# Kernel tuning notes

Hardware: AMD Instinct MI355X
Metric: run time of the kernel (lower is better)

The kernel has to match this reference:

```python
import jax, jax.numpy as jnp
import numpy as np

N, J, H, O, SD = 6144, 2000, 100, 6144, 2


def setup_inputs() -> dict:
    key = jax.random.key(0)
    ks = jax.random.split(key, 18)
    sc = lambda fan_in: 1.0 / np.sqrt(fan_in)
    inp = {
        "gene_expr": jax.random.normal(ks[0], (N, J), jnp.float32),
        "spatial_pos": jax.random.normal(ks[1], (N, SD), jnp.float32),
        # linear weights stored [in, out] (y = x @ W + b)
        "Wq": jax.random.normal(ks[2], (J, H), jnp.float32) * sc(J),
        "bq": jnp.zeros((H,), jnp.float32),
        "Wk": jax.random.normal(ks[3], (J, H), jnp.float32) * sc(J),
        "bk": jnp.zeros((H,), jnp.float32),
        "Wv": jax.random.normal(ks[4], (J, O), jnp.float32) * sc(J),
        "bv": jnp.zeros((O,), jnp.float32),
        "Ws": jax.random.normal(ks[5], (SD, H), jnp.float32) * sc(SD),
        "bs": jnp.zeros((H,), jnp.float32),
        "W1": jax.random.normal(ks[6], (H, H), jnp.float32) * sc(H),
        "b1": jnp.zeros((H,), jnp.float32),
        "W2": jax.random.normal(ks[7], (H, H), jnp.float32) * sc(H),
        "b2": jnp.zeros((H,), jnp.float32),
        "Wf": jax.random.normal(ks[8], (H, 1), jnp.float32) * sc(H),
        "bf": jnp.zeros((1,), jnp.float32),
    }
    return inp


def reference(gene_expr, spatial_pos, Wq, bq, Wk, bk, Wv, bv, Ws, bs,
              W1, b1, W2, b2, Wf, bf):
    dk = jnp.sqrt(jnp.asarray(H, gene_expr.dtype))

    Q = gene_expr @ Wq + bq            # [N,H]
    K = gene_expr @ Wk + bk            # [N,H]
    V = gene_expr @ Wv + bv            # [N,O]

    # advanced spatial scalar + pairwise tanh difference
    sp = spatial_pos @ Ws + bs                             # [N,H]
    enh = jax.nn.relu(jnp.tanh(sp @ W1 + b1) @ W2 + b2)    # [N,H]
    f = (enh @ Wf + bf)[:, 0]                              # [N]
    fdiff = jnp.tanh(f[:, None] - f[None, :])              # [N,N]

    # gaussian kernel of squared pairwise distances (cdist p=2, sigma=1)
    sq = jnp.sum(spatial_pos * spatial_pos, axis=1)
    d2 = jnp.maximum(sq[:, None] + sq[None, :] - 2.0 * (spatial_pos @ spatial_pos.T), 0.0)
    spatial_sim = jnp.exp(-d2 / 2.0)                       # [N,N]

    # row-wise cosine similarity of gene expression
    norm = jnp.linalg.norm(gene_expr, axis=1, keepdims=True)
    xn = gene_expr / jnp.maximum(norm, 1e-12)
    cos_sim = xn @ xn.T                                    # [N,N]

    logits = (Q @ K.T) / dk + spatial_sim + cos_sim + fdiff
    attn = jax.nn.softmax(logits, axis=-1)                 # stable softmax == max-subtract in src
    out = attn @ V                                         # [N,O]
    return attn, out
```

## Files before the change

### kernel.cpp

```cpp
#include <hip/hip_runtime.h>
#include <stdint.h>
#include <math.h>

#define NN 6144
#define JJ 2000
#define HH 100
#define KB 2176
#define XOFF 128
#define KQK 2048

typedef __bf16 bf16;
typedef __bf16 bf16x8 __attribute__((ext_vector_type(8)));
typedef float f32x4 __attribute__((ext_vector_type(4)));

__device__ __forceinline__ void load_lds16(const void* g, void* l) {
  __builtin_amdgcn_global_load_lds(
      (const __attribute__((address_space(1))) void*)(uintptr_t)g,
      (__attribute__((address_space(3))) void*)(uint32_t)(uintptr_t)l,
      16, 0, 0);
}

template <int MODE>
__global__ __launch_bounds__(256, 2) void gemm_bt(
    const bf16* __restrict__ A, const bf16* __restrict__ B,
    int lda, int ldb, int kdim,
    const float* __restrict__ p0, const float* __restrict__ p1,
    const float* __restrict__ p2,
    bf16* __restrict__ ob0, bf16* __restrict__ ob1,
    float* __restrict__ of0, float* __restrict__ rowsum)
{
  __shared__ alignas(16) bf16 As[128 * 64];
  __shared__ alignas(16) bf16 Bs[128 * 64];

  const int tid = threadIdx.x;
  const int lane = tid & 63;
  const int wv = tid >> 6;
  const int m0 = blockIdx.x * 128;
  const int n0 = blockIdx.y * 128;

  const int srow = lane >> 3;
  const int scol = ((lane & 7) ^ srow) * 8;
  const bf16* gA = A + (size_t)(m0 + wv * 32 + srow) * lda + scol;
  const bf16* gB = B + (size_t)(n0 + wv * 32 + srow) * ldb + scol;
  bf16* lA0 = &As[(wv * 32) * 64];
  bf16* lB0 = &Bs[(wv * 32) * 64];

  const int l15 = lane & 15;
  const int l4 = lane >> 4;
  const int s7 = l15 & 7;
  const int wm = (wv >> 1) * 64;
  const int wn = (wv & 1) * 64;
  const bf16* ra0 = &As[(wm + l15) * 64 + ((l4 ^ s7) * 8)];
  const bf16* ra1 = &As[(wm + l15) * 64 + (((l4 + 4) ^ s7) * 8)];
  const bf16* rb0 = &Bs[(wn + l15) * 64 + ((l4 ^ s7) * 8)];
  const bf16* rb1 = &Bs[(wn + l15) * 64 + (((l4 + 4) ^ s7) * 8)];

  f32x4 acc[4][4];
#pragma unroll
  for (int i = 0; i < 4; ++i)
#pragma unroll
    for (int j = 0; j < 4; ++j) acc[i][j] = {0.f, 0.f, 0.f, 0.f};

  const int kiters = kdim >> 6;
  for (int kt = 0; kt < kiters; ++kt) {
    __syncthreads();
#pragma unroll
    for (int it = 0; it < 4; ++it) {
      load_lds16(gA + (size_t)it * 8 * lda, lA0 + it * 512);
      load_lds16(gB + (size_t)it * 8 * ldb, lB0 + it * 512);
    }
    gA += 64;
    gB += 64;
    __syncthreads();
#pragma unroll
    for (int ks = 0; ks < 2; ++ks) {
      const bf16* ra = ks ? ra1 : ra0;
      const bf16* rb = ks ? rb1 : rb0;
      bf16x8 af[4], bb[4];
#pragma unroll
      for (int i = 0; i < 4; ++i)
        af[i] = *(const bf16x8*)(ra + i * 1024);
#pragma unroll
      for (int j = 0; j < 4; ++j)
        bb[j] = *(const bf16x8*)(rb + j * 1024);
#pragma unroll
      for (int i = 0; i < 4; ++i)
#pragma unroll
        for (int j = 0; j < 4; ++j)
          acc[i][j] = __builtin_amdgcn_mfma_f32_16x16x32_bf16(af[i], bb[j], acc[i][j], 0, 0, 0);
    }
  }

  const int row_base = m0 + wm + l4 * 4;
  const int col_base = n0 + wn + l15;

  if (MODE == 3) {
#pragma unroll
    for (int i = 0; i < 4; ++i) {
#pragma unroll
      for (int r = 0; r < 4; ++r) {
        int row = row_base + i * 16 + r;
        float nm = p0[row];
#pragma unroll
        for (int j = 0; j < 4; ++j) {
          int h = col_base + j * 16;
          float v = acc[i][j][r] * nm;
          if (h < HH) ob0[(size_t)row * KB + h] = (bf16)((v + p1[h]) * 0.1f);
          else if (h < 2 * HH) ob1[(size_t)row * KB + (h - HH)] = (bf16)(v + p2[h - HH]);
        }
      }
    }
  }
}

__device__ __forceinline__ void gemm192_core(
    const bf16* __restrict__ A, const bf16* __restrict__ B,
    int lda, int ldb, int kdim, int m0, int n0, f32x4 (&acc)[6][4])
{
  __shared__ alignas(16) bf16 As[2][192 * 64];
  __shared__ alignas(16) bf16 Bs[2][256 * 64];

  const int tid = threadIdx.x;
  const int lane = tid & 63;
  const int wv = tid >> 6;
  const int wm = wv >> 2;
  const int wn = wv & 3;
  const int l15 = lane & 15;
  const int l4 = lane >> 4;
  const int s7 = lane & 7;
  const int srow = lane >> 3;
  const int scol = ((lane & 7) ^ srow) * 8;

  const bf16* gA = A + (size_t)(m0 + wv * 8 + srow) * lda + scol;
  const bf16* gB = B + (size_t)(n0 + wv * 8 + srow) * ldb + scol;

  const int c0 = (l4 ^ s7) * 8;
  const int c1 = ((l4 + 4) ^ s7) * 8;

#pragma unroll
  for (int i = 0; i < 6; ++i)
#pragma unroll
    for (int j = 0; j < 4; ++j) acc[i][j] = {0.f, 0.f, 0.f, 0.f};

  const int kt = kdim >> 6;

#define STA(bufi, h, T)                                                        \
  load_lds16(gA + (size_t)((h) * 64) * lda + (size_t)(T) * 64,                 \
             &As[(bufi)][((h) * 64 + wv * 8) * 64])
#define STB(bufi, h, T)                                                        \
  load_lds16(gB + (size_t)((h) * 64) * ldb + (size_t)(T) * 64,                 \
             &Bs[(bufi)][((h) * 64 + wv * 8) * 64])

  STB(0, 0, 0); STB(0, 1, 0); STB(0, 2, 0); STB(0, 3, 0);
  STA(0, 0, 0); STA(0, 1, 0); STA(0, 2, 0);
  STB(1, 0, 1); STB(1, 1, 1);
  STA(1, 0, 1); STA(1, 1, 1); STA(1, 2, 1);
  asm volatile("s_waitcnt vmcnt(5)" ::: "memory");
  __builtin_amdgcn_s_barrier();

  bf16x8 af[3][2], b0[2][2], b1[2][2];

  for (int t2 = 0; t2 < kt; t2 += 2) {
#pragma unroll
    for (int u = 0; u < 2; ++u) {
      const int T = t2 + u;
      const int buf = u, bufn = u ^ 1;
      const bf16* pA = &As[buf][(wm * 96 + l15) * 64];
      const bf16* pB = &Bs[buf][(wn * 64 + l15) * 64];

#pragma unroll
      for (int fm = 0; fm < 3; ++fm) {
        af[fm][0] = *(const bf16x8*)(pA + (fm * 16) * 64 + c0);
        af[fm][1] = *(const bf16x8*)(pA + (fm * 16) * 64 + c1);
      }
#pragma unroll
      for (int fn = 0; fn < 2; ++fn) {
        b0[fn][0] = *(const bf16x8*)(pB + (fn * 16) * 64 + c0);
        b0[fn][1] = *(const bf16x8*)(pB + (fn * 16) * 64 + c1);
      }
      if (T + 1 < kt) { STB(bufn, 2, T + 1); STB(bufn, 3, T + 1); }
      __builtin_amdgcn_s_barrier();
      asm volatile("s_waitcnt lgkmcnt(0)" ::: "memory");
      __builtin_amdgcn_s_setprio(1);
#pragma unroll
      for (int ks = 0; ks < 2; ++ks)
#pragma unroll
        for (int fm = 0; fm < 3; ++fm)
#pragma unroll
          for (int fn = 0; fn < 2; ++fn)
            acc[fm][fn] = __builtin_amdgcn_mfma_f32_16x16x32_bf16(
                af[fm][ks], b0[fn][ks], acc[fm][fn], 0, 0, 0);
      __builtin_amdgcn_s_setprio(0);
      __builtin_amdgcn_s_barrier();

#pragma unroll
      for (int fn = 0; fn < 2; ++fn) {
        b1[fn][0] = *(const bf16x8*)(pB + ((32 + fn * 16) * 64) + c0);
        b1[fn][1] = *(const bf16x8*)(pB + ((32 + fn * 16) * 64) + c1);
      }
      __builtin_amdgcn_s_barrier();
      asm volatile("s_waitcnt lgkmcnt(0)" ::: "memory");
      __builtin_amdgcn_s_setprio(1);
#pragma unroll
      for (int ks = 0; ks < 2; ++ks)
#pragma unroll
        for (int fm = 0; fm < 3; ++fm)
#pragma unroll
          for (int fn = 0; fn < 2; ++fn)
            acc[fm][2 + fn] = __builtin_amdgcn_mfma_f32_16x16x32_bf16(
                af[fm][ks], b1[fn][ks], acc[fm][2 + fn], 0, 0, 0);
      __builtin_amdgcn_s_setprio(0);
      __builtin_amdgcn_s_barrier();

#pragma unroll
      for (int fm = 0; fm < 3; ++fm) {
        af[fm][0] = *(const bf16x8*)(pA + ((48 + fm * 16) * 64) + c0);
        af[fm][1] = *(const bf16x8*)(pA + ((48 + fm * 16) * 64) + c1);
      }
      if (T + 2 < kt) { STB(buf, 0, T + 2); STB(buf, 1, T + 2); }
      __builtin_amdgcn_s_barrier();
      asm volatile("s_waitcnt lgkmcnt(0)" ::: "memory");
      __builtin_amdgcn_s_setprio(1);
#pragma unroll
      for (int ks = 0; ks < 2; ++ks)
#pragma unroll
        for (int fm = 0; fm < 3; ++fm)
#pragma unroll
          for (int fn = 0; fn < 2; ++fn)
            acc[3 + fm][2 + fn] = __builtin_amdgcn_mfma_f32_16x16x32_bf16(
                af[fm][ks], b1[fn][ks], acc[3 + fm][2 + fn], 0, 0, 0);
      __builtin_amdgcn_s_setprio(0);
      __builtin_amdgcn_s_barrier();

      if (T + 2 < kt) { STA(buf, 0, T + 2); STA(buf, 1, T + 2); STA(buf, 2, T + 2); }
      __builtin_amdgcn_s_barrier();
      __builtin_amdgcn_s_setprio(1);
#pragma unroll
      for (int ks = 0; ks < 2; ++ks)
#pragma unroll
        for (int fm = 0; fm < 3; ++fm)
#pragma unroll
          for (int fn = 0; fn < 2; ++fn)
            acc[3 + fm][fn] = __builtin_amdgcn_mfma_f32_16x16x32_bf16(
                af[fm][ks], b0[fn][ks], acc[3 + fm][fn], 0, 0, 0);
      __builtin_amdgcn_s_setprio(0);
      if (T + 1 < kt) {
        if (T + 2 < kt) asm volatile("s_waitcnt vmcnt(5)" ::: "memory");
        else            asm volatile("s_waitcnt vmcnt(0)" ::: "memory");
      }
      __builtin_amdgcn_s_barrier();
    }
  }
#undef STA
#undef STB
}

__global__ __launch_bounds__(512, 2) void gemm256_lv(
    const bf16* __restrict__ Abig, const bf16* __restrict__ WvT,
    const bf16* __restrict__ Bbig,
    const float* __restrict__ sqv, const float* __restrict__ fv,
    const float* __restrict__ spos, const float* __restrict__ normv,
    const float* __restrict__ bv,
    bf16* __restrict__ P, bf16* __restrict__ Vt, float* __restrict__ rowsum)
{
  int lin = blockIdx.y * 32 + blockIdx.x;
  int swz = (lin & 7) * 96 + (lin >> 3);
  const int m0 = (swz & 31) * 192;
  const int n0 = (swz >> 5) * 256;
  const bool isl = (blockIdx.z == 0);

  f32x4 acc[6][4];
  gemm192_core(isl ? Abig : WvT, Bbig, KB, KB, KB, m0, n0, acc);

  const int tid = threadIdx.x;
  const int lane = tid & 63;
  const int wv = tid >> 6;
  const int wm = wv >> 2, wn = wv & 3;
  const int l15 = lane & 15, l4 = lane >> 4;
  const int row_base = m0 + wm * 96 + l4 * 4;
  const int col_base = n0 + wn * 64 + l15;

  if (isl) {
    float sqc[4], fc[4], pxc[4], pyc[4];
#pragma unroll
    for (int j = 0; j < 4; ++j) {
      int c = col_base + j * 16;
      sqc[j] = sqv[c];
      fc[j] = fv[c];
      pxc[j] = spos[2 * c];
      pyc[j] = spos[2 * c + 1];
    }
#pragma unroll
    for (int i = 0; i < 6; ++i) {
#pragma unroll
      for (int r = 0; r < 4; ++r) {
        int row = row_base + i * 16 + r;
        float sqr = sqv[row], fr = fv[row];
        float pxr = spos[2 * row], pyr = spos[2 * row + 1];
        float rs = 0.f;
#pragma unroll
        for (int j = 0; j < 4; ++j) {
          int c = col_base + j * 16;
          float d2 = fmaxf(sqr + sqc[j] - 2.f * (pxr * pxc[j] + pyr * pyc[j]), 0.f);
          float lg = acc[i][j][r] + __expf(-0.5f * d2) + tanhf(fr - fc[j]);
          float e = __expf(lg);
          P[(size_t)row * NN + c] = (bf16)e;
          rs += e;
        }
        rs += __shfl_xor(rs, 1);
        rs += __shfl_xor(rs, 2);
        rs += __shfl_xor(rs, 4);
        rs += __shfl_xor(rs, 8);
        if (l15 == 0) atomicAdd(&rowsum[row], rs);
      }
    }
  } else {
    float nc[4];
#pragma unroll
    for (int j = 0; j < 4; ++j) nc[j] = normv[col_base + j * 16];
#pragma unroll
    for (int i = 0; i < 6; ++i) {
#pragma unroll
      for (int r = 0; r < 4; ++r) {
        int row = row_base + i * 16 + r;
        float bvr = bv[row];
#pragma unroll
        for (int j = 0; j < 4; ++j)
          Vt[(size_t)row * NN + col_base + j * 16] = (bf16)(acc[i][j][r] * nc[j] + bvr);
      }
    }
  }
}

__global__ __launch_bounds__(512, 2) void gemm256_pv(
    const bf16* __restrict__ Pm, const bf16* __restrict__ Vt,
    const float* __restrict__ rowsum, float* __restrict__ outp)
{
  int lin = blockIdx.y * 32 + blockIdx.x;
  int swz = (lin & 7) * 96 + (lin >> 3);
  const int m0 = (swz & 31) * 192;
  const int n0 = (swz >> 5) * 256;

  f32x4 acc[6][4];
  gemm192_core(Pm, Vt, NN, NN, NN, m0, n0, acc);

  const int tid = threadIdx.x;
  const int lane = tid & 63;
  const int wv = tid >> 6;
  const int wm = wv >> 2, wn = wv & 3;
  const int l15 = lane & 15, l4 = lane >> 4;
  const int row_base = m0 + wm * 96 + l4 * 4;
  const int col_base = n0 + wn * 64 + l15;
#pragma unroll
  for (int i = 0; i < 6; ++i) {
#pragma unroll
    for (int r = 0; r < 4; ++r) {
      int row = row_base + i * 16 + r;
      float rinv = 1.f / rowsum[row];
#pragma unroll
      for (int j = 0; j < 4; ++j)
        outp[(size_t)row * NN + col_base + j * 16] = acc[i][j][r] * rinv;
    }
  }
}

__global__ void prep_xn(const float* __restrict__ gene, bf16* __restrict__ Ab,
                        bf16* __restrict__ Bb, float* __restrict__ normv)
{
  int row = blockIdx.x, tid = threadIdx.x;
  const float* g = gene + (size_t)row * JJ;
  float s = 0.f;
  for (int k = tid; k < JJ; k += 256) { float v = g[k]; s += v * v; }
#pragma unroll
  for (int m = 32; m >= 1; m >>= 1) s += __shfl_xor(s, m);
  __shared__ float red[4];
  if ((tid & 63) == 0) red[tid >> 6] = s;
  __syncthreads();
  float tot = red[0] + red[1] + red[2] + red[3];
  float nrm = sqrtf(tot);
  float rinv = 1.f / fmaxf(nrm, 1e-12f);
  if (tid == 0) normv[row] = nrm;
  bf16* a = Ab + (size_t)row * KB;
  bf16* b = Bb + (size_t)row * KB;
  for (int k = tid; k < JJ; k += 256) {
    bf16 v = (bf16)(g[k] * rinv);
    a[XOFF + k] = v;
    b[XOFF + k] = v;
  }
  if (tid < 28) { a[HH + tid] = (bf16)0.f; b[HH + tid] = (bf16)0.f; }
  if (tid < 48) { a[XOFF + JJ + tid] = (bf16)0.f; b[XOFF + JJ + tid] = (bf16)0.f; }
}

__global__ void prep_sf(const float* __restrict__ spos,
                        const float* __restrict__ Ws, const float* __restrict__ bs,
                        const float* __restrict__ W1, const float* __restrict__ b1,
                        const float* __restrict__ W2, const float* __restrict__ b2,
                        const float* __restrict__ Wf, const float* __restrict__ bfp,
                        float* __restrict__ sqv, float* __restrict__ fv)
{
  int row = blockIdx.x, tid = threadIdx.x;
  float px = spos[2 * row], py = spos[2 * row + 1];
  if (tid == 0) sqv[row] = px * px + py * py;
  __shared__ float sp[HH], t1[HH], e2[HH];
  if (tid < HH) sp[tid] = px * Ws[tid] + py * Ws[HH + tid] + bs[tid];
  __syncthreads();
  if (tid < HH) {
    float s = b1[tid];
    for (int gi = 0; gi < HH; ++gi) s += sp[gi] * W1[gi * HH + tid];
    t1[tid] = tanhf(s);
  }
  __syncthreads();
  if (tid < HH) {
    float s = b2[tid];
    for (int gi = 0; gi < HH; ++gi) s += t1[gi] * W2[gi * HH + tid];
    e2[tid] = fmaxf(s, 0.f) * Wf[tid];
  }
  __syncthreads();
  if (tid < 64) {
    float s = e2[tid] + ((tid < 36) ? e2[tid + 64] : 0.f);
#pragma unroll
    for (int m = 32; m >= 1; m >>= 1) s += __shfl_xor(s, m);
    if (tid == 0) fv[row] = s + bfp[0];
  }
}

__global__ void pack_wqk(const float* __restrict__ Wq, const float* __restrict__ Wk,
                         bf16* __restrict__ Wt)
{
  int idx = blockIdx.x * 256 + threadIdx.x;
  int h = idx >> 11;
  int k = idx & 2047;
  float v = 0.f;
  if (k < JJ) {
    if (h < HH) v = Wq[(size_t)k * HH + h];
    else if (h < 2 * HH) v = Wk[(size_t)k * HH + (h - HH)];
  }
  Wt[idx] = (bf16)v;
}

__global__ void pack_wvt(const float* __restrict__ Wv, bf16* __restrict__ Wt)
{
  __shared__ float tile[32][33];
  int tx = threadIdx.x & 31, ty = threadIdx.x >> 5;
  int o0 = blockIdx.x * 32, j0 = blockIdx.y * 32;
#pragma unroll
  for (int rr = 0; rr < 32; rr += 8) {
    int j = j0 + ty + rr;
    tile[ty + rr][tx] = (j < JJ) ? Wv[(size_t)j * NN + o0 + tx] : 0.f;
  }
  __syncthreads();
#pragma unroll
  for (int rr = 0; rr < 32; rr += 8) {
    int o = o0 + ty + rr;
    Wt[(size_t)o * KB + XOFF + j0 + tx] = (bf16)tile[tx][ty + rr];
  }
}

__global__ void zero_wvt_head(bf16* __restrict__ Wt)
{
  int idx = blockIdx.x * 256 + threadIdx.x;
  int o = idx >> 7, c = idx & 127;
  Wt[(size_t)o * KB + c] = (bf16)0.f;
}

__global__ void norm_attn(const bf16* __restrict__ P, const float* __restrict__ rowsum,
                          float* __restrict__ attn)
{
  int row = blockIdx.x;
  float rinv = 1.f / rowsum[row];
  const bf16x8* p = (const bf16x8*)(P + (size_t)row * NN);
  float* dst = attn + (size_t)row * NN;
  for (int c = threadIdx.x; c < NN / 8; c += 256) {
    bf16x8 v = p[c];
#pragma unroll
    for (int e = 0; e < 8; ++e) dst[c * 8 + e] = (float)v[e] * rinv;
  }
}

extern "C" void kernel_launch(void* const* d_in, const int* in_sizes, int n_in,
                              void* d_out, int out_size, void* d_ws, size_t ws_size,
                              hipStream_t stream)
{
  const float* gene = (const float*)d_in[0];
  const float* spos = (const float*)d_in[1];
  const float* Wq = (const float*)d_in[2];
  const float* bq = (const float*)d_in[3];
  const float* Wk = (const float*)d_in[4];
  const float* bk = (const float*)d_in[5];
  const float* Wv = (const float*)d_in[6];
  const float* bv = (const float*)d_in[7];
  const float* Ws = (const float*)d_in[8];
  const float* bs = (const float*)d_in[9];
  const float* W1 = (const float*)d_in[10];
  const float* b1 = (const float*)d_in[11];
  const float* W2 = (const float*)d_in[12];
  const float* b2 = (const float*)d_in[13];
  const float* Wf = (const float*)d_in[14];
  const float* bfp = (const float*)d_in[15];

  char* ws = (char*)d_ws;
  bf16* Abig = (bf16*)ws;            ws += (size_t)NN * KB * 2;
  bf16* Bbig = (bf16*)ws;            ws += (size_t)NN * KB * 2;
  bf16* WvT  = (bf16*)ws;            ws += (size_t)NN * KB * 2;
  bf16* WqkT = (bf16*)ws;            ws += (size_t)256 * KQK * 2;
  bf16* P    = (bf16*)ws;            ws += (size_t)NN * NN * 2;
  float* rowsum = (float*)ws;        ws += (size_t)NN * 4;
  float* normv  = (float*)ws;        ws += (size_t)NN * 4;
  float* sqv    = (float*)ws;        ws += (size_t)NN * 4;
  float* fv     = (float*)ws;        ws += (size_t)NN * 4;

  float* attn = (float*)d_out;
  float* outp = (float*)d_out + (size_t)NN * NN;
  bf16* Vt = (bf16*)d_out;

  hipMemsetAsync(rowsum, 0, NN * sizeof(float), stream);
  prep_xn<<<NN, 256, 0, stream>>>(gene, Abig, Bbig, normv);
  prep_sf<<<NN, 128, 0, stream>>>(spos, Ws, bs, W1, b1, W2, b2, Wf, bfp, sqv, fv);
  pack_wqk<<<(256 * KQK) / 256, 256, 0, stream>>>(Wq, Wk, WqkT);
  pack_wvt<<<dim3(NN / 32, KQK / 32), 256, 0, stream>>>(Wv, WvT);
  zero_wvt_head<<<(NN * XOFF) / 256, 256, 0, stream>>>(WvT);

  gemm_bt<3><<<dim3(NN / 128, 2), 256, 0, stream>>>(
      Abig + XOFF, WqkT, KB, KQK, KQK, normv, bq, bk, Abig, Bbig, nullptr, nullptr);
  gemm256_lv<<<dim3(32, 24, 2), 512, 0, stream>>>(
      Abig, WvT, Bbig, sqv, fv, spos, normv, bv, P, Vt, rowsum);
  gemm256_pv<<<dim3(32, 24), 512, 0, stream>>>(P, Vt, rowsum, outp);
  norm_attn<<<NN, 256, 0, stream>>>(P, rowsum, attn);
}
```

Baseline: 1.223 ms.

## Restructure gemm192 main loop into two phases and use nontemporal output stores

```diff
diff --git a/kernel.cpp b/kernel.cpp
--- a/kernel.cpp
+++ b/kernel.cpp
@@ -151,14 +151,13 @@
   load_lds16(gB + (size_t)((h) * 64) * ldb + (size_t)(T) * 64,                 \
              &Bs[(bufi)][((h) * 64 + wv * 8) * 64])
 
+  STA(0, 0, 0); STA(0, 1, 0); STA(0, 2, 0);
   STB(0, 0, 0); STB(0, 1, 0); STB(0, 2, 0); STB(0, 3, 0);
-  STA(0, 0, 0); STA(0, 1, 0); STA(0, 2, 0);
-  STB(1, 0, 1); STB(1, 1, 1);
-  STA(1, 0, 1); STA(1, 1, 1); STA(1, 2, 1);
-  asm volatile("s_waitcnt vmcnt(5)" ::: "memory");
+  STB(1, 0, 1); STB(1, 1, 1); STB(1, 2, 1); STB(1, 3, 1);
+  asm volatile("s_waitcnt vmcnt(4)" ::: "memory");
   __builtin_amdgcn_s_barrier();
 
-  bf16x8 af[3][2], b0[2][2], b1[2][2];
+  bf16x8 af[6][2], b0[2][2], b1[2][2];
 
   for (int t2 = 0; t2 < kt; t2 += 2) {
 #pragma unroll
@@ -169,7 +168,7 @@
       const bf16* pB = &Bs[buf][(wn * 64 + l15) * 64];
 
 #pragma unroll
-      for (int fm = 0; fm < 3; ++fm) {
+      for (int fm = 0; fm < 6; ++fm) {
         af[fm][0] = *(const bf16x8*)(pA + (fm * 16) * 64 + c0);
         af[fm][1] = *(const bf16x8*)(pA + (fm * 16) * 64 + c1);
       }
@@ -177,75 +176,37 @@
       for (int fn = 0; fn < 2; ++fn) {
         b0[fn][0] = *(const bf16x8*)(pB + (fn * 16) * 64 + c0);
         b0[fn][1] = *(const bf16x8*)(pB + (fn * 16) * 64 + c1);
-      }
-      if (T + 1 < kt) { STB(bufn, 2, T + 1); STB(bufn, 3, T + 1); }
-      __builtin_amdgcn_s_barrier();
-      asm volatile("s_waitcnt lgkmcnt(0)" ::: "memory");
+        b1[fn][0] = *(const bf16x8*)(pB + ((32 + fn * 16) * 64) + c0);
+        b1[fn][1] = *(const bf16x8*)(pB + ((32 + fn * 16) * 64) + c1);
+      }
+      if (T + 1 < kt) { STA(bufn, 0, T + 1); STA(bufn, 1, T + 1); STA(bufn, 2, T + 1); }
       __builtin_amdgcn_s_setprio(1);
 #pragma unroll
       for (int ks = 0; ks < 2; ++ks)
 #pragma unroll
-        for (int fm = 0; fm < 3; ++fm)
+        for (int fm = 0; fm < 6; ++fm)
 #pragma unroll
           for (int fn = 0; fn < 2; ++fn)
             acc[fm][fn] = __builtin_amdgcn_mfma_f32_16x16x32_bf16(
                 af[fm][ks], b0[fn][ks], acc[fm][fn], 0, 0, 0);
       __builtin_amdgcn_s_setprio(0);
+      asm volatile("s_waitcnt lgkmcnt(0)" ::: "memory");
       __builtin_amdgcn_s_barrier();
 
-#pragma unroll
-      for (int fn = 0; fn < 2; ++fn) {
-        b1[fn][0] = *(const bf16x8*)(pB + ((32 + fn * 16) * 64) + c0);
-        b1[fn][1] = *(const bf16x8*)(pB + ((32 + fn * 16) * 64) + c1);
-      }
-      __builtin_amdgcn_s_barrier();
-      asm volatile("s_waitcnt lgkmcnt(0)" ::: "memory");
+      if (T + 2 < kt) { STB(buf, 0, T + 2); STB(buf, 1, T + 2);
+                        STB(buf, 2, T + 2); STB(buf, 3, T + 2); }
       __builtin_amdgcn_s_setprio(1);
 #pragma unroll
       for (int ks = 0; ks < 2; ++ks)
 #pragma unroll
-        for (int fm = 0; fm < 3; ++fm)
+        for (int fm = 0; fm < 6; ++fm)
 #pragma unroll
           for (int fn = 0; fn < 2; ++fn)
             acc[fm][2 + fn] = __builtin_amdgcn_mfma_f32_16x16x32_bf16(
                 af[fm][ks], b1[fn][ks], acc[fm][2 + fn], 0, 0, 0);
       __builtin_amdgcn_s_setprio(0);
-      __builtin_amdgcn_s_barrier();
-
-#pragma unroll
-      for (int fm = 0; fm < 3; ++fm) {
-        af[fm][0] = *(const bf16x8*)(pA + ((48 + fm * 16) * 64) + c0);
-        af[fm][1] = *(const bf16x8*)(pA + ((48 + fm * 16) * 64) + c1);
-      }
-      if (T + 2 < kt) { STB(buf, 0, T + 2); STB(buf, 1, T + 2); }
-      __builtin_amdgcn_s_barrier();
-      asm volatile("s_waitcnt lgkmcnt(0)" ::: "memory");
-      __builtin_amdgcn_s_setprio(1);
-#pragma unroll
-      for (int ks = 0; ks < 2; ++ks)
-#pragma unroll
-        for (int fm = 0; fm < 3; ++fm)
-#pragma unroll
-          for (int fn = 0; fn < 2; ++fn)
-            acc[3 + fm][2 + fn] = __builtin_amdgcn_mfma_f32_16x16x32_bf16(
-                af[fm][ks], b1[fn][ks], acc[3 + fm][2 + fn], 0, 0, 0);
-      __builtin_amdgcn_s_setprio(0);
-      __builtin_amdgcn_s_barrier();
-
-      if (T + 2 < kt) { STA(buf, 0, T + 2); STA(buf, 1, T + 2); STA(buf, 2, T + 2); }
-      __builtin_amdgcn_s_barrier();
-      __builtin_amdgcn_s_setprio(1);
-#pragma unroll
-      for (int ks = 0; ks < 2; ++ks)
-#pragma unroll
-        for (int fm = 0; fm < 3; ++fm)
-#pragma unroll
-          for (int fn = 0; fn < 2; ++fn)
-            acc[3 + fm][fn] = __builtin_amdgcn_mfma_f32_16x16x32_bf16(
-                af[fm][ks], b0[fn][ks], acc[3 + fm][fn], 0, 0, 0);
-      __builtin_amdgcn_s_setprio(0);
       if (T + 1 < kt) {
-        if (T + 2 < kt) asm volatile("s_waitcnt vmcnt(5)" ::: "memory");
+        if (T + 2 < kt) asm volatile("s_waitcnt vmcnt(4)" ::: "memory");
         else            asm volatile("s_waitcnt vmcnt(0)" ::: "memory");
       }
       __builtin_amdgcn_s_barrier();
@@ -359,7 +320,8 @@
       float rinv = 1.f / rowsum[row];
 #pragma unroll
       for (int j = 0; j < 4; ++j)
-        outp[(size_t)row * NN + col_base + j * 16] = acc[i][j][r] * rinv;
+        __builtin_nontemporal_store(acc[i][j][r] * rinv,
+                                    &outp[(size_t)row * NN + col_base + j * 16]);
     }
   }
 }
@@ -473,7 +435,8 @@
   for (int c = threadIdx.x; c < NN / 8; c += 256) {
     bf16x8 v = p[c];
 #pragma unroll
-    for (int e = 0; e < 8; ++e) dst[c * 8 + e] = (float)v[e] * rinv;
+    for (int e = 0; e < 8; ++e)
+      __builtin_nontemporal_store((float)v[e] * rinv, &dst[c * 8 + e]);
   }
 }
 
```

Measured after the change: 1.188 ms. 2.9% less time.
